# Kernel optimization log

Hardware: AMD Instinct MI355X
Metric: run time of the kernel (lower is better)

## Reference

```python
import jax, jax.numpy as jnp
import numpy as np

N, E, G = 50000, 500000, 1
NODE_F, EDGE_F, GLOB_F = 7, 3, 2
LATENT = 128
HIDDEN = 128
STEPS = 2
OUT = 3
LN_EPS = 1e-6


def _mlp2(x, W0, b0, W1, b1):
    # flax MLP with feature_sizes=[hidden, latent]: Dense+gelu, Dense
    return jax.nn.gelu(x @ W0 + b0) @ W1 + b1


def _ln(x, scale, bias):
    # flax nn.LayerNorm over last axis, eps=1e-6
    m = jnp.mean(x, axis=-1, keepdims=True)
    v = jnp.mean(jnp.square(x - m), axis=-1, keepdims=True)
    return (x - m) * jax.lax.rsqrt(v + LN_EPS) * scale + bias


def setup_inputs() -> dict:
    key = jax.random.key(0)
    ks = iter(jax.random.split(key, 40))

    def nrm(shape, scale=0.05):
        return jax.random.normal(next(ks), shape, jnp.float32) * scale

    return {
        "nodes": jax.random.normal(next(ks), (N, NODE_F), jnp.float32),
        "edges": jax.random.normal(next(ks), (E, EDGE_F), jnp.float32),
        "globals_": jax.random.normal(next(ks), (G, GLOB_F), jnp.float32),
        "senders": jax.random.randint(next(ks), (E,), 0, N, jnp.int32),
        "receivers": jax.random.randint(next(ks), (E,), 0, N, jnp.int32),
        "ne_W0": nrm((NODE_F, HIDDEN)), "ne_b0": jnp.zeros((HIDDEN,), jnp.float32),
        "ne_W1": nrm((HIDDEN, LATENT)), "ne_b1": jnp.zeros((LATENT,), jnp.float32),
        "ee_W0": nrm((EDGE_F, HIDDEN)), "ee_b0": jnp.zeros((HIDDEN,), jnp.float32),
        "ee_W1": nrm((HIDDEN, LATENT)), "ee_b1": jnp.zeros((LATENT,), jnp.float32),
        "eu_W0": nrm((STEPS, 3 * LATENT + GLOB_F, HIDDEN)), "eu_b0": jnp.zeros((STEPS, HIDDEN), jnp.float32),
        "eu_W1": nrm((STEPS, HIDDEN, LATENT)), "eu_b1": jnp.zeros((STEPS, LATENT), jnp.float32),
        "nu_W0": nrm((STEPS, 2 * LATENT + GLOB_F, HIDDEN)), "nu_b0": jnp.zeros((STEPS, HIDDEN), jnp.float32),
        "nu_W1": nrm((STEPS, HIDDEN, LATENT)), "nu_b1": jnp.zeros((STEPS, LATENT), jnp.float32),
        "ln_scale": jnp.ones((LATENT,), jnp.float32), "ln_bias": jnp.zeros((LATENT,), jnp.float32),
        "dec_W0": nrm((LATENT, HIDDEN)), "dec_b0": jnp.zeros((HIDDEN,), jnp.float32),
        "dec_W1": nrm((HIDDEN, OUT)), "dec_b1": jnp.zeros((OUT,), jnp.float32),
    }


def reference(nodes, edges, globals_, senders, receivers,
              ne_W0, ne_b0, ne_W1, ne_b1,
              ee_W0, ee_b0, ee_W1, ee_b1,
              eu_W0, eu_b0, eu_W1, eu_b1,
              nu_W0, nu_b0, nu_W1, nu_b1,
              ln_scale, ln_bias,
              dec_W0, dec_b0, dec_W1, dec_b1):
    # embed nodes and edges
    nh = _mlp2(nodes, ne_W0, ne_b0, ne_W1, ne_b1)   # [N, LATENT]
    eh = _mlp2(edges, ee_W0, ee_b0, ee_W1, ee_b1)   # [E, LATENT]
    g_e = jnp.broadcast_to(globals_, (E, GLOB_F))   # single graph -> broadcast
    g_n = jnp.broadcast_to(globals_, (N, GLOB_F))
    for s in range(STEPS):
        # edge update: concat(edges, sender_feats, receiver_feats, globals)
        edge_in = jnp.concatenate([eh, nh[senders], nh[receivers], g_e], axis=-1)
        new_e = _mlp2(edge_in, eu_W0[s], eu_b0[s], eu_W1[s], eu_b1[s])
        # jraph aggregate: received_attributes = segment_sum over receivers
        received = jax.ops.segment_sum(new_e, receivers, num_segments=N)
        # node update: concat(nodes, received, globals) (sent attrs unused)
        node_in = jnp.concatenate([nh, received, g_n], axis=-1)
        new_n = _mlp2(node_in, nu_W0[s], nu_b0[s], nu_W1[s], nu_b1[s])
        # skip connections then shared LayerNorm on nodes and edges
        nh = _ln(nh + new_n, ln_scale, ln_bias)
        eh = _ln(eh + new_e, ln_scale, ln_bias)
    # decode node features to output_dim=3
    return _mlp2(nh, dec_W0, dec_b0, dec_W1, dec_b1)  # [N, 3]
```

## Files before the change

### kernel.cpp

```cpp
#include <hip/hip_runtime.h>
#include <hip/hip_bf16.h>


typedef __bf16 bf16;
typedef __attribute__((ext_vector_type(8))) __bf16 bf16x8;
typedef __attribute__((ext_vector_type(2))) __bf16 bf16x2;
typedef __attribute__((ext_vector_type(4))) float f32x4;

__device__ __forceinline__ float gelu_t(float x) {
    const float kn0 = -1.5957691216057308f;
    const float kn1 = -0.07135481627159855f;
    float x2 = x * x;
    float w = x * __builtin_fmaf(kn1, x2, kn0);
    float e = __expf(w);
    return __fdividef(x, 1.0f + e);
}

struct PackDesc { const float* src; int Kcopy; int dstOff; };
struct PackArgs { PackDesc d[13]; };

__global__ __launch_bounds__(256) void pack_all_kernel(PackArgs pa, bf16* dst, int total) {
    int i = blockIdx.x * 256 + threadIdx.x;
    if (i >= total) return;
    int s = 0;
#pragma unroll
    for (int j = 1; j < 13; ++j) if (i >= pa.d[j].dstOff) s = j;
    int local = i - pa.d[s].dstOff;
    int k = local >> 7, n = local & 127;
    float v = (k < pa.d[s].Kcopy) ? pa.d[s].src[(size_t)k * 128 + n] : 0.0f;
    dst[pa.d[s].dstOff + ((k >> 3) * 128 + n) * 8 + (k & 7)] = (bf16)v;
}

__global__ void fold_bias_kernel(const float* g, const float* euW0, const float* eub0,
                                 const float* nuW0, const float* nub0,
                                 float* eu_eff, float* nu_eff) {
    int t = threadIdx.x;
    if (t < 128) {
        float g0 = g[0], g1 = g[1];
#pragma unroll
        for (int s = 0; s < 2; ++s) {
            eu_eff[s * 128 + t] = eub0[s * 128 + t]
                + g0 * euW0[((size_t)s * 386 + 384) * 128 + t]
                + g1 * euW0[((size_t)s * 386 + 385) * 128 + t];
            nu_eff[s * 128 + t] = nub0[s * 128 + t]
                + g0 * nuW0[((size_t)s * 258 + 256) * 128 + t]
                + g1 * nuW0[((size_t)s * 258 + 257) * 128 + t];
        }
    }
}

__global__ __launch_bounds__(256) void zero_kernel(float4* p, int n4) {
    int i = blockIdx.x * 256 + threadIdx.x;
    if (i < n4) p[i] = float4{0.0f, 0.0f, 0.0f, 0.0f};
}

__global__ __launch_bounds__(256) void hist_kernel(const int* __restrict__ recv,
                                                   int* __restrict__ deg, int E) {
    int e = blockIdx.x * 256 + threadIdx.x;
    if (e < E) atomicAdd(&deg[recv[e]], 1);
}

__global__ __launch_bounds__(256) void scan_part_kernel(const int* __restrict__ deg,
                                                        int* __restrict__ cursor,
                                                        int* __restrict__ bsum, int n) {
    __shared__ int tmp[256];
    int t = threadIdx.x, g = blockIdx.x * 256 + t;
    int v = (g < n) ? deg[g] : 0;
    tmp[t] = v; __syncthreads();
#pragma unroll
    for (int o = 1; o < 256; o <<= 1) {
        int x = (t >= o) ? tmp[t - o] : 0;
        __syncthreads();
        tmp[t] += x;
        __syncthreads();
    }
    if (g < n) cursor[g] = tmp[t] - v;
    if (t == 255) bsum[blockIdx.x] = tmp[255];
}

__global__ void scan_top_kernel(int* bsum, int nb) {
    __shared__ int tmp[256];
    int t = threadIdx.x;
    int v = (t < nb) ? bsum[t] : 0;
    tmp[t] = v; __syncthreads();
#pragma unroll
    for (int o = 1; o < 256; o <<= 1) {
        int x = (t >= o) ? tmp[t - o] : 0;
        __syncthreads();
        tmp[t] += x;
        __syncthreads();
    }
    if (t < nb) bsum[t] = tmp[t] - v;
}

__global__ __launch_bounds__(256) void scan_add_kernel(int* __restrict__ cursor,
                                                       const int* __restrict__ bsum, int n) {
    int g = blockIdx.x * 256 + threadIdx.x;
    if (g < n) cursor[g] += bsum[blockIdx.x];
}

__global__ __launch_bounds__(256) void scatter_kernel(
    const int* __restrict__ send, const int* __restrict__ recv,
    const float* __restrict__ edges_raw, int* __restrict__ cursor,
    float* __restrict__ edges_s, int* __restrict__ sendp, int* __restrict__ recvp, int E) {
    int e = blockIdx.x * 256 + threadIdx.x;
    if (e >= E) return;
    int r = recv[e];
    int pos = atomicAdd(&cursor[r], 1);
    sendp[pos] = send[e]; recvp[pos] = r;
    edges_s[(size_t)pos * 3]     = edges_raw[(size_t)e * 3];
    edges_s[(size_t)pos * 3 + 1] = edges_raw[(size_t)e * 3 + 1];
    edges_s[(size_t)pos * 3 + 2] = edges_raw[(size_t)e * 3 + 2];
}

__global__ __launch_bounds__(256) void segsum_kernel(const bf16* __restrict__ newe,
                                                     const int* __restrict__ endoff,
                                                     bf16* __restrict__ recvb, int N) {
    int node = blockIdx.x * 4 + (threadIdx.x >> 6);
    if (node >= N) return;
    int lane = threadIdx.x & 63;
    int start = (node == 0) ? 0 : endoff[node - 1];
    int end = endoff[node];
    float s0 = 0.0f, s1 = 0.0f, t0 = 0.0f, t1 = 0.0f;
    int e = start;
    for (; e + 1 < end; e += 2) {
        bf16x2 v = *(const bf16x2*)(newe + (size_t)e * 128 + lane * 2);
        bf16x2 u = *(const bf16x2*)(newe + (size_t)(e + 1) * 128 + lane * 2);
        s0 += (float)v[0]; s1 += (float)v[1];
        t0 += (float)u[0]; t1 += (float)u[1];
    }
    if (e < end) {
        bf16x2 v = *(const bf16x2*)(newe + (size_t)e * 128 + lane * 2);
        s0 += (float)v[0]; s1 += (float)v[1];
    }
    bf16x2 o; o[0] = (bf16)(s0 + t0); o[1] = (bf16)(s1 + t1);
    *(bf16x2*)(recvb + (size_t)node * 128 + lane * 2) = o;
}

template <int STEP>
__global__ __launch_bounds__(256, 5) void edge_kernel(
    const float* __restrict__ edges_s,
    const int* __restrict__ sendp, const int* __restrict__ recvp,
    const bf16* __restrict__ nh_b, bf16* __restrict__ newe,
    const bf16* __restrict__ We0, const float* __restrict__ be0,
    const bf16* __restrict__ We1, const float* __restrict__ be1,
    const float* __restrict__ ln_s, const float* __restrict__ ln_b,
    const bf16* __restrict__ Ws0, const float* __restrict__ bs0,
    const bf16* __restrict__ Ws1, const float* __restrict__ bs1,
    int E)
{
    __shared__ __align__(16) bf16 Hsep[4 * 16 * 136];
    const int tid = threadIdx.x, lane = tid & 63, w = tid >> 6;
    const int n16 = lane & 15, quad = lane >> 4;
    const int m0 = blockIdx.x * 64;
    int m = m0 + w * 16 + n16; if (m >= E) m = E - 1;
    const int sIdx = sendp[m], rIdx = recvp[m];

    bf16* Hw = &Hsep[w * 16 * 136];
    const f32x4 z = {0.0f, 0.0f, 0.0f, 0.0f};
    f32x4 acc[8];

#pragma unroll
    for (int t = 0; t < 8; ++t) acc[t] = z;
    {
        bf16x8 a;
#pragma unroll
        for (int j = 0; j < 8; ++j) a[j] = (bf16)0.0f;
        if (quad == 0) {
            a[0] = (bf16)edges_s[(size_t)m * 3];
            a[1] = (bf16)edges_s[(size_t)m * 3 + 1];
            a[2] = (bf16)edges_s[(size_t)m * 3 + 2];
        }
        const bf16* bp = We0 + ((size_t)(quad * 128 + n16)) * 8;
#pragma unroll
        for (int t = 0; t < 8; ++t) {
            bf16x8 b = *(const bf16x8*)(bp + t * 128);
            acc[t] = __builtin_amdgcn_mfma_f32_16x16x32_bf16(a, b, acc[t], 0, 0, 0);
        }
    }
#pragma unroll
    for (int t = 0; t < 8; ++t) {
        float bb = be0[t * 16 + n16];
#pragma unroll
        for (int r = 0; r < 4; ++r)
            Hw[(quad * 4 + r) * 136 + t * 16 + n16] = (bf16)gelu_t(acc[t][r] + bb);
    }
#pragma unroll
    for (int t = 0; t < 8; ++t) acc[t] = z;
#pragma unroll
    for (int kc = 0; kc < 128; kc += 32) {
        bf16x8 a = *(const bf16x8*)&Hw[n16 * 136 + kc + quad * 8];
        const bf16* bp = We1 + ((size_t)(((kc >> 3) + quad) * 128 + n16)) * 8;
#pragma unroll
        for (int t = 0; t < 8; ++t) {
            bf16x8 b = *(const bf16x8*)(bp + t * 128);
            acc[t] = __builtin_amdgcn_mfma_f32_16x16x32_bf16(a, b, acc[t], 0, 0, 0);
        }
    }
#pragma unroll
    for (int t = 0; t < 8; ++t) {
        float bb = be1[t * 16 + n16];
#pragma unroll
        for (int r = 0; r < 4; ++r)
            Hw[(quad * 4 + r) * 136 + t * 16 + n16] = (bf16)(acc[t][r] + bb);
    }
    bf16x8 a1[4];
#pragma unroll
    for (int c = 0; c < 4; ++c)
        a1[c] = *(const bf16x8*)&Hw[n16 * 136 + c * 32 + quad * 8];

    if constexpr (STEP == 1) {
        float x[4][8];
        float sm = 0.0f, sq = 0.0f;
#pragma unroll
        for (int c = 0; c < 4; ++c) {
            bf16x8 ne = *(const bf16x8*)(newe + (size_t)m * 128 + c * 32 + quad * 8);
#pragma unroll
            for (int j = 0; j < 8; ++j) {
                float v = (float)a1[c][j] + (float)ne[j];
                x[c][j] = v; sm += v; sq += v * v;
            }
        }
        sm += __shfl_xor(sm, 16); sq += __shfl_xor(sq, 16);
        sm += __shfl_xor(sm, 32); sq += __shfl_xor(sq, 32);
        float mean = sm * (1.0f / 128.0f);
        float inv = rsqrtf(sq * (1.0f / 128.0f) - mean * mean + 1e-6f);
#pragma unroll
        for (int c = 0; c < 4; ++c)
#pragma unroll
            for (int j = 0; j < 8; ++j) {
                int col = c * 32 + quad * 8 + j;
                a1[c][j] = (bf16)((x[c][j] - mean) * inv * ln_s[col] + ln_b[col]);
            }
    }

#pragma unroll
    for (int t = 0; t < 8; ++t) acc[t] = z;
#pragma unroll
    for (int c = 0; c < 12; ++c) {
        const int k0 = (c & 3) * 32 + quad * 8;
        bf16x8 af;
        if (c < 4)      af = a1[c];
        else if (c < 8) af = *(const bf16x8*)(nh_b + (size_t)sIdx * 128 + k0);
        else            af = *(const bf16x8*)(nh_b + (size_t)rIdx * 128 + k0);
        const bf16* bp = Ws0 + ((size_t)((c * 4 + quad) * 128 + n16)) * 8;
#pragma unroll
        for (int t = 0; t < 8; ++t) {
            bf16x8 b = *(const bf16x8*)(bp + t * 128);
            acc[t] = __builtin_amdgcn_mfma_f32_16x16x32_bf16(af, b, acc[t], 0, 0, 0);
        }
    }
#pragma unroll
    for (int t = 0; t < 8; ++t) {
        float bb = bs0[t * 16 + n16];
#pragma unroll
        for (int r = 0; r < 4; ++r)
            Hw[(quad * 4 + r) * 136 + t * 16 + n16] = (bf16)gelu_t(acc[t][r] + bb);
    }
#pragma unroll
    for (int t = 0; t < 8; ++t) acc[t] = z;
#pragma unroll
    for (int kc = 0; kc < 128; kc += 32) {
        bf16x8 a = *(const bf16x8*)&Hw[n16 * 136 + kc + quad * 8];
        const bf16* bp = Ws1 + ((size_t)(((kc >> 3) + quad) * 128 + n16)) * 8;
#pragma unroll
        for (int t = 0; t < 8; ++t) {
            bf16x8 b = *(const bf16x8*)(bp + t * 128);
            acc[t] = __builtin_amdgcn_mfma_f32_16x16x32_bf16(a, b, acc[t], 0, 0, 0);
        }
    }
#pragma unroll
    for (int t = 0; t < 8; ++t) {
        float bb = bs1[t * 16 + n16];
#pragma unroll
        for (int r = 0; r < 4; ++r) {
            int row = m0 + w * 16 + quad * 4 + r;
            if (row < E)
                newe[(size_t)row * 128 + t * 16 + n16] = (bf16)(acc[t][r] + bb);
        }
    }
}

template <int MODE, int K1, int RAWF>
__global__ __launch_bounds__(256, 5) void mlp2_kernel(
    const void* __restrict__ Araw0v, const bf16* __restrict__ Araw1b,
    const bf16* __restrict__ W0p, const float* __restrict__ b0,
    const bf16* __restrict__ W1p, const float* __restrict__ b1,
    const float* __restrict__ ln_s, const float* __restrict__ ln_b,
    void* out0v, int Mtotal)
{
    __shared__ __align__(16) bf16 Hsep[(MODE == 4) ? 1 : (4 * 16 * 136)];

    const int tid = threadIdx.x, lane = tid & 63, w = tid >> 6;
    const int n16 = lane & 15, quad = lane >> 4;
    const int m0 = blockIdx.x * 64;

    const float* Araw0f = (const float*)Araw0v;
    const bf16*  Araw0b = (const bf16*)Araw0v;
    float* out0f = (float*)out0v;
    bf16*  out0b = (bf16*)out0v;

    int m = m0 + w * 16 + n16;
    if (m >= Mtotal) m = Mtotal - 1;

    const f32x4 z = {0.0f, 0.0f, 0.0f, 0.0f};
    f32x4 acc[8];
#pragma unroll
    for (int t = 0; t < 8; ++t) acc[t] = z;

#pragma unroll
    for (int c = 0; c < K1 / 32; ++c) {
        const int k0 = c * 32 + quad * 8;
        bf16x8 a;
        if constexpr (MODE == 3) {
            if (c < 4) a = *(const bf16x8*)(Araw0b + (size_t)m * 128 + k0);
            else       a = *(const bf16x8*)(Araw1b + (size_t)m * 128 + (k0 - 128));
        } else if constexpr (MODE == 4) {
            a = *(const bf16x8*)(Araw0b + (size_t)m * 128 + k0);
        } else {
#pragma unroll
            for (int j = 0; j < 8; ++j) a[j] = (bf16)0.0f;
            if (quad == 0) {
#pragma unroll
                for (int j = 0; j < RAWF; ++j)
                    a[j] = (bf16)Araw0f[(size_t)m * RAWF + j];
            }
        }
        const bf16* bp = W0p + ((size_t)((c * 4 + quad) * 128 + n16)) * 8;
#pragma unroll
        for (int t = 0; t < 8; ++t) {
            bf16x8 b = *(const bf16x8*)(bp + t * 128);
            acc[t] = __builtin_amdgcn_mfma_f32_16x16x32_bf16(a, b, acc[t], 0, 0, 0);
        }
    }

    float b0v[8];
#pragma unroll
    for (int t = 0; t < 8; ++t) b0v[t] = b0[t * 16 + n16];

    if constexpr (MODE == 4) {
        const float* W1d = ln_s;
        const float* b1d = ln_b;
        float p[4][3];
#pragma unroll
        for (int r = 0; r < 4; ++r) { p[r][0] = 0; p[r][1] = 0; p[r][2] = 0; }
#pragma unroll
        for (int t = 0; t < 8; ++t) {
            int col = t * 16 + n16;
            float w0 = W1d[col * 3 + 0], w1 = W1d[col * 3 + 1], w2 = W1d[col * 3 + 2];
#pragma unroll
            for (int r = 0; r < 4; ++r) {
                float h = gelu_t(acc[t][r] + b0v[t]);
                p[r][0] += h * w0; p[r][1] += h * w1; p[r][2] += h * w2;
            }
        }
#pragma unroll
        for (int mm = 1; mm < 16; mm <<= 1)
#pragma unroll
            for (int r = 0; r < 4; ++r) {
                p[r][0] += __shfl_xor(p[r][0], mm);
                p[r][1] += __shfl_xor(p[r][1], mm);
                p[r][2] += __shfl_xor(p[r][2], mm);
            }
        if (n16 < 3) {
            float bb = b1d[n16];
#pragma unroll
            for (int r = 0; r < 4; ++r) {
                int row = m0 + w * 16 + quad * 4 + r;
                if (row < Mtotal)
                    out0f[(size_t)row * 3 + n16] = p[r][n16] + bb;
            }
        }
        return;
    }

    bf16* Hw = &Hsep[w * 16 * 136];
#pragma unroll
    for (int t = 0; t < 8; ++t)
#pragma unroll
        for (int r = 0; r < 4; ++r)
            Hw[(quad * 4 + r) * 136 + t * 16 + n16] = (bf16)gelu_t(acc[t][r] + b0v[t]);

#pragma unroll
    for (int t = 0; t < 8; ++t) acc[t] = z;
#pragma unroll
    for (int kc = 0; kc < 128; kc += 32) {
        bf16x8 a = *(const bf16x8*)&Hw[n16 * 136 + kc + quad * 8];
        const bf16* bp = W1p + ((size_t)(((kc >> 3) + quad) * 128 + n16)) * 8;
#pragma unroll
        for (int t = 0; t < 8; ++t) {
            bf16x8 b = *(const bf16x8*)(bp + t * 128);
            acc[t] = __builtin_amdgcn_mfma_f32_16x16x32_bf16(a, b, acc[t], 0, 0, 0);
        }
    }

    if constexpr (MODE == 0) {
#pragma unroll
        for (int t = 0; t < 8; ++t) {
            float b1v = b1[t * 16 + n16];
#pragma unroll
            for (int r = 0; r < 4; ++r) {
                int row = m0 + w * 16 + quad * 4 + r;
                if (row < Mtotal)
                    out0b[(size_t)row * 128 + t * 16 + n16] = (bf16)(acc[t][r] + b1v);
            }
        }
        return;
    }

    float b1v[8], scl[8], bia[8];
#pragma unroll
    for (int t = 0; t < 8; ++t) {
        int col = t * 16 + n16;
        b1v[t] = b1[col]; scl[t] = ln_s[col]; bia[t] = ln_b[col];
    }
    int rowg[4];
#pragma unroll
    for (int r = 0; r < 4; ++r) rowg[r] = m0 + w * 16 + quad * 4 + r;
    float x[8][4];
    float sm[4] = {0, 0, 0, 0}, sq[4] = {0, 0, 0, 0};
#pragma unroll
    for (int t = 0; t < 8; ++t) {
        int col = t * 16 + n16;
#pragma unroll
        for (int r = 0; r < 4; ++r) {
            bool ok = rowg[r] < Mtotal;
            float v = acc[t][r] + b1v[t];
            float old = ok ? (float)Araw0b[(size_t)rowg[r] * 128 + col] : 0.0f;
            float xx = old + v;
            x[t][r] = xx; sm[r] += xx; sq[r] += xx * xx;
        }
    }
#pragma unroll
    for (int mm = 1; mm < 16; mm <<= 1)
#pragma unroll
        for (int r = 0; r < 4; ++r) {
            sm[r] += __shfl_xor(sm[r], mm);
            sq[r] += __shfl_xor(sq[r], mm);
        }
    float mean[4], inv[4];
#pragma unroll
    for (int r = 0; r < 4; ++r) {
        mean[r] = sm[r] * (1.0f / 128.0f);
        float var = sq[r] * (1.0f / 128.0f) - mean[r] * mean[r];
        inv[r] = rsqrtf(var + 1e-6f);
    }
#pragma unroll
    for (int t = 0; t < 8; ++t)
#pragma unroll
        for (int r = 0; r < 4; ++r)
            if (rowg[r] < Mtotal)
                out0b[(size_t)rowg[r] * 128 + t * 16 + n16] =
                    (bf16)((x[t][r] - mean[r]) * inv[r] * scl[t] + bia[t]);
}

extern "C" void kernel_launch(void* const* d_in, const int* in_sizes, int n_in,
                              void* d_out, int out_size, void* d_ws, size_t ws_size,
                              hipStream_t stream) {
    const float* nodes   = (const float*)d_in[0];
    const float* edges   = (const float*)d_in[1];
    const float* glob    = (const float*)d_in[2];
    const int*   senders = (const int*)d_in[3];
    const int*   recvrs  = (const int*)d_in[4];
    const float* ne_W0 = (const float*)d_in[5],  *ne_b0 = (const float*)d_in[6];
    const float* ne_W1 = (const float*)d_in[7],  *ne_b1 = (const float*)d_in[8];
    const float* ee_W0 = (const float*)d_in[9],  *ee_b0 = (const float*)d_in[10];
    const float* ee_W1 = (const float*)d_in[11], *ee_b1 = (const float*)d_in[12];
    const float* eu_W0 = (const float*)d_in[13], *eu_b0 = (const float*)d_in[14];
    const float* eu_W1 = (const float*)d_in[15], *eu_b1 = (const float*)d_in[16];
    const float* nu_W0 = (const float*)d_in[17], *nu_b0 = (const float*)d_in[18];
    const float* nu_W1 = (const float*)d_in[19], *nu_b1 = (const float*)d_in[20];
    const float* ln_s  = (const float*)d_in[21], *ln_b  = (const float*)d_in[22];
    const float* dc_W0 = (const float*)d_in[23], *dc_b0 = (const float*)d_in[24];
    const float* dc_W1 = (const float*)d_in[25], *dc_b1 = (const float*)d_in[26];

    const int N = 50000, E = 500000;

    const int KD[13] = {32, 128, 32, 128, 384, 384, 128, 128, 256, 256, 128, 128, 128};
    const int KC[13] = {7, 128, 3, 128, 384, 384, 128, 128, 256, 256, 128, 128, 128};
    int pre[14]; pre[0] = 0;
    for (int i = 0; i < 13; ++i) pre[i + 1] = pre[i] + KD[i] * 128;
    const int totalPack = pre[13];

    char* ws = (char*)d_ws;
    size_t off = 0;
    auto alloc = [&](size_t bytes) -> char* {
        char* p = ws + off;
        off = (off + bytes + 255) & ~(size_t)255;
        return p;
    };
    bf16*  Wp      = (bf16*)alloc((size_t)totalPack * 2);
    float* b0e_eu  = (float*)alloc(2 * 128 * 4);
    float* b0e_nu  = (float*)alloc(2 * 128 * 4);
    bf16*  nh_b    = (bf16*)alloc((size_t)N * 128 * 2);
    bf16*  recvb   = (bf16*)alloc((size_t)N * 128 * 2);
    bf16*  newe    = (bf16*)alloc((size_t)E * 128 * 2);
    int*   deg     = (int*)alloc((size_t)N * 4);
    int*   cursor  = (int*)alloc((size_t)N * 4);
    int*   bsum    = (int*)alloc(256 * 4);
    float* edges_s = (float*)alloc((size_t)E * 3 * 4);
    int*   sendp   = (int*)alloc((size_t)E * 4);
    int*   recvp   = (int*)alloc((size_t)E * 4);

    if (off > ws_size) return;

    PackArgs pa;
    const float* srcs[13] = {
        ne_W0, ne_W1, ee_W0, ee_W1,
        eu_W0, eu_W0 + (size_t)386 * 128,
        eu_W1, eu_W1 + (size_t)128 * 128,
        nu_W0, nu_W0 + (size_t)258 * 128,
        nu_W1, nu_W1 + (size_t)128 * 128,
        dc_W0};
    for (int i = 0; i < 13; ++i) { pa.d[i].src = srcs[i]; pa.d[i].Kcopy = KC[i]; pa.d[i].dstOff = pre[i]; }

    pack_all_kernel<<<(totalPack + 255) / 256, 256, 0, stream>>>(pa, Wp, totalPack);
    fold_bias_kernel<<<1, 128, 0, stream>>>(glob, eu_W0, eu_b0, nu_W0, nu_b0, b0e_eu, b0e_nu);

    const int gEdge = (E + 255) / 256;
    const int nb = (N + 255) / 256;
    zero_kernel<<<(N / 4 + 255) / 256, 256, 0, stream>>>((float4*)deg, N / 4);
    hist_kernel<<<gEdge, 256, 0, stream>>>(recvrs, deg, E);
    scan_part_kernel<<<nb, 256, 0, stream>>>(deg, cursor, bsum, N);
    scan_top_kernel<<<1, 256, 0, stream>>>(bsum, nb);
    scan_add_kernel<<<nb, 256, 0, stream>>>(cursor, bsum, N);
    scatter_kernel<<<gEdge, 256, 0, stream>>>(senders, recvrs, edges, cursor,
                                              edges_s, sendp, recvp, E);

    const int gN = (N + 63) / 64, gE = (E + 63) / 64;
    mlp2_kernel<0, 32, 7><<<gN, 256, 0, stream>>>(
        nodes, nullptr, Wp + pre[0], ne_b0, Wp + pre[1], ne_b1,
        nullptr, nullptr, nh_b, N);

    for (int s = 0; s < 2; ++s) {
        if (s == 0)
            edge_kernel<0><<<gE, 256, 0, stream>>>(
                edges_s, sendp, recvp, nh_b, newe,
                Wp + pre[2], ee_b0, Wp + pre[3], ee_b1, ln_s, ln_b,
                Wp + pre[4], b0e_eu, Wp + pre[6], eu_b1, E);
        else
            edge_kernel<1><<<gE, 256, 0, stream>>>(
                edges_s, sendp, recvp, nh_b, newe,
                Wp + pre[2], ee_b0, Wp + pre[3], ee_b1, ln_s, ln_b,
                Wp + pre[5], b0e_eu + 128, Wp + pre[7], eu_b1 + 128, E);
        segsum_kernel<<<(N + 3) / 4, 256, 0, stream>>>(newe, cursor, recvb, N);
        mlp2_kernel<3, 256, 0><<<gN, 256, 0, stream>>>(
            nh_b, recvb, Wp + pre[8 + s], b0e_nu + s * 128,
            Wp + pre[10 + s], nu_b1 + s * 128, ln_s, ln_b, nh_b, N);
    }

    mlp2_kernel<4, 128, 0><<<gN, 256, 0, stream>>>(
        nh_b, nullptr, Wp + pre[12], dc_b0, nullptr, nullptr,
        dc_W1, dc_b1, d_out, N);
}
```

Measured before the change: 808.7 us.

## Fuse decoder into final node update and vectorize segment sum

The second-step node-update kernel now also runs the decoder MLP on the LayerNorm output held in shared memory. It writes the 3-wide output directly, which removes a separate decoder launch and the re-read of node latents. The segment-sum kernel now has each quarter-wavefront read a full 128-wide edge row with 8-wide bf16 loads, striding over edges, then reduces across groups with shuffles. Launch bounds occupancy drops from 5 to 4 to make room for the extra registers, and every mode now allocates full shared memory.

```diff
diff --git a/kernel.cpp b/kernel.cpp
--- a/kernel.cpp
+++ b/kernel.cpp
@@ -119,22 +119,26 @@
     int node = blockIdx.x * 4 + (threadIdx.x >> 6);
     if (node >= N) return;
     int lane = threadIdx.x & 63;
+    int g = lane >> 4, cl = lane & 15;
     int start = (node == 0) ? 0 : endoff[node - 1];
     int end = endoff[node];
-    float s0 = 0.0f, s1 = 0.0f, t0 = 0.0f, t1 = 0.0f;
-    int e = start;
-    for (; e + 1 < end; e += 2) {
-        bf16x2 v = *(const bf16x2*)(newe + (size_t)e * 128 + lane * 2);
-        bf16x2 u = *(const bf16x2*)(newe + (size_t)(e + 1) * 128 + lane * 2);
-        s0 += (float)v[0]; s1 += (float)v[1];
-        t0 += (float)u[0]; t1 += (float)u[1];
-    }
-    if (e < end) {
-        bf16x2 v = *(const bf16x2*)(newe + (size_t)e * 128 + lane * 2);
-        s0 += (float)v[0]; s1 += (float)v[1];
-    }
-    bf16x2 o; o[0] = (bf16)(s0 + t0); o[1] = (bf16)(s1 + t1);
-    *(bf16x2*)(recvb + (size_t)node * 128 + lane * 2) = o;
+    float s[8] = {0, 0, 0, 0, 0, 0, 0, 0};
+    for (int e = start + g; e < end; e += 4) {
+        bf16x8 v = *(const bf16x8*)(newe + (size_t)e * 128 + cl * 8);
+#pragma unroll
+        for (int j = 0; j < 8; ++j) s[j] += (float)v[j];
+    }
+#pragma unroll
+    for (int j = 0; j < 8; ++j) {
+        s[j] += __shfl_xor(s[j], 16);
+        s[j] += __shfl_xor(s[j], 32);
+    }
+    if (g == 0) {
+        bf16x8 o;
+#pragma unroll
+        for (int j = 0; j < 8; ++j) o[j] = (bf16)s[j];
+        *(bf16x8*)(recvb + (size_t)node * 128 + cl * 8) = o;
+    }
 }
 
 template <int STEP>
@@ -282,14 +286,16 @@
 }
 
 template <int MODE, int K1, int RAWF>
-__global__ __launch_bounds__(256, 5) void mlp2_kernel(
+__global__ __launch_bounds__(256, 4) void mlp2_kernel(
     const void* __restrict__ Araw0v, const bf16* __restrict__ Araw1b,
     const bf16* __restrict__ W0p, const float* __restrict__ b0,
     const bf16* __restrict__ W1p, const float* __restrict__ b1,
     const float* __restrict__ ln_s, const float* __restrict__ ln_b,
+    const bf16* __restrict__ Wd0, const float* __restrict__ db0,
+    const float* __restrict__ dW1, const float* __restrict__ db1,
     void* out0v, int Mtotal)
 {
-    __shared__ __align__(16) bf16 Hsep[(MODE == 4) ? 1 : (4 * 16 * 136)];
+    __shared__ __align__(16) bf16 Hsep[4 * 16 * 136];
 
     const int tid = threadIdx.x, lane = tid & 63, w = tid >> 6;
     const int n16 = lane & 15, quad = lane >> 4;
@@ -312,11 +318,9 @@
     for (int c = 0; c < K1 / 32; ++c) {
         const int k0 = c * 32 + quad * 8;
         bf16x8 a;
-        if constexpr (MODE == 3) {
+        if constexpr (MODE == 3 || MODE == 5) {
             if (c < 4) a = *(const bf16x8*)(Araw0b + (size_t)m * 128 + k0);
             else       a = *(const bf16x8*)(Araw1b + (size_t)m * 128 + (k0 - 128));
-        } else if constexpr (MODE == 4) {
-            a = *(const bf16x8*)(Araw0b + (size_t)m * 128 + k0);
         } else {
 #pragma unroll
             for (int j = 0; j < 8; ++j) a[j] = (bf16)0.0f;
@@ -338,19 +342,120 @@
 #pragma unroll
     for (int t = 0; t < 8; ++t) b0v[t] = b0[t * 16 + n16];
 
-    if constexpr (MODE == 4) {
-        const float* W1d = ln_s;
-        const float* b1d = ln_b;
+    bf16* Hw = &Hsep[w * 16 * 136];
+#pragma unroll
+    for (int t = 0; t < 8; ++t)
+#pragma unroll
+        for (int r = 0; r < 4; ++r)
+            Hw[(quad * 4 + r) * 136 + t * 16 + n16] = (bf16)gelu_t(acc[t][r] + b0v[t]);
+
+#pragma unroll
+    for (int t = 0; t < 8; ++t) acc[t] = z;
+#pragma unroll
+    for (int kc = 0; kc < 128; kc += 32) {
+        bf16x8 a = *(const bf16x8*)&Hw[n16 * 136 + kc + quad * 8];
+        const bf16* bp = W1p + ((size_t)(((kc >> 3) + quad) * 128 + n16)) * 8;
+#pragma unroll
+        for (int t = 0; t < 8; ++t) {
+            bf16x8 b = *(const bf16x8*)(bp + t * 128);
+            acc[t] = __builtin_amdgcn_mfma_f32_16x16x32_bf16(a, b, acc[t], 0, 0, 0);
+        }
+    }
+
+    if constexpr (MODE == 0) {
+#pragma unroll
+        for (int t = 0; t < 8; ++t) {
+            float b1v = b1[t * 16 + n16];
+#pragma unroll
+            for (int r = 0; r < 4; ++r) {
+                int row = m0 + w * 16 + quad * 4 + r;
+                if (row < Mtotal)
+                    out0b[(size_t)row * 128 + t * 16 + n16] = (bf16)(acc[t][r] + b1v);
+            }
+        }
+        return;
+    }
+
+    float b1v[8], scl[8], bia[8];
+#pragma unroll
+    for (int t = 0; t < 8; ++t) {
+        int col = t * 16 + n16;
+        b1v[t] = b1[col]; scl[t] = ln_s[col]; bia[t] = ln_b[col];
+    }
+    int rowg[4];
+#pragma unroll
+    for (int r = 0; r < 4; ++r) rowg[r] = m0 + w * 16 + quad * 4 + r;
+    float x[8][4];
+    float sm[4] = {0, 0, 0, 0}, sq[4] = {0, 0, 0, 0};
+#pragma unroll
+    for (int t = 0; t < 8; ++t) {
+        int col = t * 16 + n16;
+#pragma unroll
+        for (int r = 0; r < 4; ++r) {
+            bool ok = rowg[r] < Mtotal;
+            float v = acc[t][r] + b1v[t];
+            float old = ok ? (float)Araw0b[(size_t)rowg[r] * 128 + col] : 0.0f;
+            float xx = old + v;
+            x[t][r] = xx; sm[r] += xx; sq[r] += xx * xx;
+        }
+    }
+#pragma unroll
+    for (int mm = 1; mm < 16; mm <<= 1)
+#pragma unroll
+        for (int r = 0; r < 4; ++r) {
+            sm[r] += __shfl_xor(sm[r], mm);
+            sq[r] += __shfl_xor(sq[r], mm);
+        }
+    float mean[4], inv[4];
+#pragma unroll
+    for (int r = 0; r < 4; ++r) {
+        mean[r] = sm[r] * (1.0f / 128.0f);
+        float var = sq[r] * (1.0f / 128.0f) - mean[r] * mean[r];
+        inv[r] = rsqrtf(var + 1e-6f);
+    }
+
+    if constexpr (MODE == 3) {
+#pragma unroll
+        for (int t = 0; t < 8; ++t)
+#pragma unroll
+            for (int r = 0; r < 4; ++r)
+                if (rowg[r] < Mtotal)
+                    out0b[(size_t)rowg[r] * 128 + t * 16 + n16] =
+                        (bf16)((x[t][r] - mean[r]) * inv[r] * scl[t] + bia[t]);
+        return;
+    }
+
+#pragma unroll
+    for (int t = 0; t < 8; ++t)
+#pragma unroll
+        for (int r = 0; r < 4; ++r)
+            Hw[(quad * 4 + r) * 136 + t * 16 + n16] =
+                (bf16)((x[t][r] - mean[r]) * inv[r] * scl[t] + bia[t]);
+
+#pragma unroll
+    for (int t = 0; t < 8; ++t) acc[t] = z;
+#pragma unroll
+    for (int kc = 0; kc < 128; kc += 32) {
+        bf16x8 a = *(const bf16x8*)&Hw[n16 * 136 + kc + quad * 8];
+        const bf16* bp = Wd0 + ((size_t)(((kc >> 3) + quad) * 128 + n16)) * 8;
+#pragma unroll
+        for (int t = 0; t < 8; ++t) {
+            bf16x8 b = *(const bf16x8*)(bp + t * 128);
+            acc[t] = __builtin_amdgcn_mfma_f32_16x16x32_bf16(a, b, acc[t], 0, 0, 0);
+        }
+    }
+    {
         float p[4][3];
 #pragma unroll
         for (int r = 0; r < 4; ++r) { p[r][0] = 0; p[r][1] = 0; p[r][2] = 0; }
 #pragma unroll
         for (int t = 0; t < 8; ++t) {
             int col = t * 16 + n16;
-            float w0 = W1d[col * 3 + 0], w1 = W1d[col * 3 + 1], w2 = W1d[col * 3 + 2];
+            float bb = db0[col];
+            float w0 = dW1[col * 3 + 0], w1 = dW1[col * 3 + 1], w2 = dW1[col * 3 + 2];
 #pragma unroll
             for (int r = 0; r < 4; ++r) {
-                float h = gelu_t(acc[t][r] + b0v[t]);
+                float h = gelu_t(acc[t][r] + bb);
                 p[r][0] += h * w0; p[r][1] += h * w1; p[r][2] += h * w2;
             }
         }
@@ -363,95 +468,13 @@
                 p[r][2] += __shfl_xor(p[r][2], mm);
             }
         if (n16 < 3) {
-            float bb = b1d[n16];
-#pragma unroll
-            for (int r = 0; r < 4; ++r) {
-                int row = m0 + w * 16 + quad * 4 + r;
-                if (row < Mtotal)
-                    out0f[(size_t)row * 3 + n16] = p[r][n16] + bb;
-            }
-        }
-        return;
-    }
-
-    bf16* Hw = &Hsep[w * 16 * 136];
-#pragma unroll
-    for (int t = 0; t < 8; ++t)
-#pragma unroll
-        for (int r = 0; r < 4; ++r)
-            Hw[(quad * 4 + r) * 136 + t * 16 + n16] = (bf16)gelu_t(acc[t][r] + b0v[t]);
-
-#pragma unroll
-    for (int t = 0; t < 8; ++t) acc[t] = z;
-#pragma unroll
-    for (int kc = 0; kc < 128; kc += 32) {
-        bf16x8 a = *(const bf16x8*)&Hw[n16 * 136 + kc + quad * 8];
-        const bf16* bp = W1p + ((size_t)(((kc >> 3) + quad) * 128 + n16)) * 8;
-#pragma unroll
-        for (int t = 0; t < 8; ++t) {
-            bf16x8 b = *(const bf16x8*)(bp + t * 128);
-            acc[t] = __builtin_amdgcn_mfma_f32_16x16x32_bf16(a, b, acc[t], 0, 0, 0);
-        }
-    }
-
-    if constexpr (MODE == 0) {
-#pragma unroll
-        for (int t = 0; t < 8; ++t) {
-            float b1v = b1[t * 16 + n16];
-#pragma unroll
-            for (int r = 0; r < 4; ++r) {
-                int row = m0 + w * 16 + quad * 4 + r;
-                if (row < Mtotal)
-                    out0b[(size_t)row * 128 + t * 16 + n16] = (bf16)(acc[t][r] + b1v);
-            }
-        }
-        return;
-    }
-
-    float b1v[8], scl[8], bia[8];
-#pragma unroll
-    for (int t = 0; t < 8; ++t) {
-        int col = t * 16 + n16;
-        b1v[t] = b1[col]; scl[t] = ln_s[col]; bia[t] = ln_b[col];
-    }
-    int rowg[4];
-#pragma unroll
-    for (int r = 0; r < 4; ++r) rowg[r] = m0 + w * 16 + quad * 4 + r;
-    float x[8][4];
-    float sm[4] = {0, 0, 0, 0}, sq[4] = {0, 0, 0, 0};
-#pragma unroll
-    for (int t = 0; t < 8; ++t) {
-        int col = t * 16 + n16;
-#pragma unroll
-        for (int r = 0; r < 4; ++r) {
-            bool ok = rowg[r] < Mtotal;
-            float v = acc[t][r] + b1v[t];
-            float old = ok ? (float)Araw0b[(size_t)rowg[r] * 128 + col] : 0.0f;
-            float xx = old + v;
-            x[t][r] = xx; sm[r] += xx; sq[r] += xx * xx;
-        }
-    }
-#pragma unroll
-    for (int mm = 1; mm < 16; mm <<= 1)
-#pragma unroll
-        for (int r = 0; r < 4; ++r) {
-            sm[r] += __shfl_xor(sm[r], mm);
-            sq[r] += __shfl_xor(sq[r], mm);
-        }
-    float mean[4], inv[4];
-#pragma unroll
-    for (int r = 0; r < 4; ++r) {
-        mean[r] = sm[r] * (1.0f / 128.0f);
-        float var = sq[r] * (1.0f / 128.0f) - mean[r] * mean[r];
-        inv[r] = rsqrtf(var + 1e-6f);
-    }
-#pragma unroll
-    for (int t = 0; t < 8; ++t)
-#pragma unroll
-        for (int r = 0; r < 4; ++r)
-            if (rowg[r] < Mtotal)
-                out0b[(size_t)rowg[r] * 128 + t * 16 + n16] =
-                    (bf16)((x[t][r] - mean[r]) * inv[r] * scl[t] + bia[t]);
+            float bb = db1[n16];
+#pragma unroll
+            for (int r = 0; r < 4; ++r)
+                if (rowg[r] < Mtotal)
+                    out0f[(size_t)rowg[r] * 3 + n16] = p[r][n16] + bb;
+        }
+    }
 }
 
 extern "C" void kernel_launch(void* const* d_in, const int* in_sizes, int n_in,
@@ -530,7 +553,7 @@
     const int gN = (N + 63) / 64, gE = (E + 63) / 64;
     mlp2_kernel<0, 32, 7><<<gN, 256, 0, stream>>>(
         nodes, nullptr, Wp + pre[0], ne_b0, Wp + pre[1], ne_b1,
-        nullptr, nullptr, nh_b, N);
+        nullptr, nullptr, nullptr, nullptr, nullptr, nullptr, nh_b, N);
 
     for (int s = 0; s < 2; ++s) {
         if (s == 0)
@@ -544,12 +567,15 @@
                 Wp + pre[2], ee_b0, Wp + pre[3], ee_b1, ln_s, ln_b,
                 Wp + pre[5], b0e_eu + 128, Wp + pre[7], eu_b1 + 128, E);
         segsum_kernel<<<(N + 3) / 4, 256, 0, stream>>>(newe, cursor, recvb, N);
-        mlp2_kernel<3, 256, 0><<<gN, 256, 0, stream>>>(
-            nh_b, recvb, Wp + pre[8 + s], b0e_nu + s * 128,
-            Wp + pre[10 + s], nu_b1 + s * 128, ln_s, ln_b, nh_b, N);
-    }
-
-    mlp2_kernel<4, 128, 0><<<gN, 256, 0, stream>>>(
-        nh_b, nullptr, Wp + pre[12], dc_b0, nullptr, nullptr,
-        dc_W1, dc_b1, d_out, N);
-}
+        if (s == 0)
+            mlp2_kernel<3, 256, 0><<<gN, 256, 0, stream>>>(
+                nh_b, recvb, Wp + pre[8], b0e_nu,
+                Wp + pre[10], nu_b1, ln_s, ln_b,
+                nullptr, nullptr, nullptr, nullptr, nh_b, N);
+        else
+            mlp2_kernel<5, 256, 0><<<gN, 256, 0, stream>>>(
+                nh_b, recvb, Wp + pre[9], b0e_nu + 128,
+                Wp + pre[11], nu_b1 + 128, ln_s, ln_b,
+                Wp + pre[12], dc_b0, dc_W1, dc_b1, d_out, N);
+    }
+}
```

Result: faster. 760.7 us (-5.9%).
